# Kernel optimization log

Measured on AMD Instinct MI355X. Metric: run time of the kernel, lower is better.

## Reference

```python
import jax, jax.numpy as jnp
import numpy as np

NUM_HEAD = 16
HEAD_DIM = 64
D_MODEL = 1024


def setup_inputs() -> dict:
    key = jax.random.key(0)
    k_x, k_q, k_k, k_v, k_o, k_ob = jax.random.split(key, 6)
    B, T, D = 2, 2048, D_MODEL
    s = 1.0 / np.sqrt(D)
    return {
        "x": jax.random.normal(k_x, (B, T, D), dtype=jnp.float32),
        "Wq": jax.random.normal(k_q, (D, D), dtype=jnp.float32) * s,
        "Wk": jax.random.normal(k_k, (D, D), dtype=jnp.float32) * s,
        "Wv": jax.random.normal(k_v, (D, D), dtype=jnp.float32) * s,
        "Wo": jax.random.normal(k_o, (D, D), dtype=jnp.float32) * s,
        "bo": jax.random.normal(k_ob, (D,), dtype=jnp.float32) * 0.01,
    }


def reference(x, Wq, Wk, Wv, Wo, bo):
    B, T, D = x.shape
    H, Dh = NUM_HEAD, HEAD_DIM
    # Faithful to the source: W_query output is named `keys`, W_key output `queries`.
    keys = x @ Wq.T
    queries = x @ Wk.T
    values = x @ Wv.T
    # [B, T, D] -> [B, H, T, Dh]
    q = queries.reshape(B, T, H, Dh).transpose(0, 2, 1, 3)
    k = keys.reshape(B, T, H, Dh).transpose(0, 2, 1, 3)
    v = values.reshape(B, T, H, Dh).transpose(0, 2, 1, 3)
    scores = jnp.einsum("bhqd,bhkd->bhqk", q, k)
    causal = jnp.triu(jnp.ones((T, T), dtype=bool), k=1)  # True above diagonal -> masked
    scores = jnp.where(causal, -jnp.inf, scores)
    weights = jax.nn.softmax(scores / np.sqrt(Dh), axis=-1)
    # dropout p=0.0 (eval): identity
    ctx = jnp.einsum("bhqk,bhkd->bhqd", weights, v)
    ctx = ctx.transpose(0, 2, 1, 3).reshape(B, T, D)
    return ctx @ Wo.T + bo
```

## Files before the change

kernel.cpp:

```cpp
#include <hip/hip_runtime.h>

#define TT 2048
#define DD 1024
#define NH 16
#define DH 64
#define MR 4096

typedef __attribute__((ext_vector_type(8))) short bf16x8;
typedef __attribute__((ext_vector_type(4))) short bf16x4;
typedef __attribute__((ext_vector_type(4))) float f32x4;
typedef __attribute__((ext_vector_type(2))) unsigned int u32x2;

__device__ __forceinline__ float bf2f(unsigned short u) {
  unsigned int x = ((unsigned int)u) << 16;
  return __builtin_bit_cast(float, x);
}
__device__ __forceinline__ unsigned short f2bf(float f) {
  unsigned int x = __builtin_bit_cast(unsigned int, f);
  x = (x + 0x7fffu + ((x >> 16) & 1u)) >> 16;
  return (unsigned short)x;
}
__device__ __forceinline__ unsigned int pack_bf2(float a, float b) {
#if __has_builtin(__builtin_amdgcn_cvt_pk_bf16_f32)
  typedef __attribute__((ext_vector_type(2))) __bf16 bf2_t;
  bf2_t v = __builtin_amdgcn_cvt_pk_bf16_f32(a, b);
  return __builtin_bit_cast(unsigned int, v);
#else
  return (unsigned int)f2bf(a) | ((unsigned int)f2bf(b) << 16);
#endif
}
__device__ __forceinline__ bf16x8 load8(const float* p) {
  bf16x8 r;
#pragma unroll
  for (int e = 0; e < 8; ++e) r[e] = (short)f2bf(p[e]);
  return r;
}

#if __has_builtin(__builtin_amdgcn_mfma_f32_16x16x16_bf16)
#define MFMA_K16(A, B, C) __builtin_amdgcn_mfma_f32_16x16x16_bf16(A, B, C, 0, 0, 0)
#else
#define MFMA_K16(A, B, C) __builtin_amdgcn_mfma_f32_16x16x16bf16_1k(A, B, C, 0, 0, 0)
#endif

__device__ __forceinline__ void stage16(const unsigned short* g,
                                        unsigned short* lbase, int lane) {
#if __has_builtin(__builtin_amdgcn_global_load_lds)
  __builtin_amdgcn_global_load_lds(
      (const __attribute__((address_space(1))) unsigned int*)g,
      (__attribute__((address_space(3))) unsigned int*)(lbase + lane * 8),
      16, 0, 0);
#else
  *(bf16x8*)(lbase + lane * 8) = *(const bf16x8*)g;
#endif
}

__global__ __launch_bounds__(256) void cvt_all(
    const float* __restrict__ Wq, const float* __restrict__ Wk,
    const float* __restrict__ Wv, const float* __restrict__ Wo,
    const float* __restrict__ x,
    unsigned short* __restrict__ Wb, unsigned short* __restrict__ xb)
{
  int c = blockIdx.x * 256 + threadIdx.x;
  if (c < 524288) {
    int idx = c * 8, n = idx >> 10, col = idx & 1023;
    const float* src = (n < 1024) ? Wk + (size_t)n * 1024
                     : (n < 2048) ? Wq + (size_t)(n - 1024) * 1024
                     : (n < 3072) ? Wv + (size_t)(n - 2048) * 1024
                                  : Wo + (size_t)(n - 3072) * 1024;
    *(bf16x8*)&Wb[idx] = load8(src + col);
  } else {
    size_t idx = (size_t)(c - 524288) * 8;
    *(bf16x8*)&xb[idx] = load8(&x[idx]);
  }
}

template <bool FAST>
__global__ __launch_bounds__(256) void gemm_qkv(
    const float* __restrict__ x, const unsigned short* __restrict__ xb,
    const unsigned short* __restrict__ Wb,
    unsigned short* __restrict__ Q, unsigned short* __restrict__ Kb,
    unsigned short* __restrict__ Vt)
{
  __shared__ unsigned short pool[8704];
  unsigned short* As = pool;
  unsigned short* Bs = pool + 4096;

  const int tid = threadIdx.x, wave = tid >> 6, lane = tid & 63;
  const int lr = lane & 15, quad = lane >> 4;
  const int bm = blockIdx.x * 128, bn = blockIdx.y * 128;
  const int wm = (wave >> 1) * 64, wn = (wave & 1) * 64;

  f32x4 acc[4][4] = {};

  for (int k0 = 0; k0 < 1024; k0 += 32) {
#pragma unroll
    for (int i = 0; i < 2; ++i) {
      int c = wave * 128 + i * 64 + lane;
      int row = c >> 2, l8 = (c & 3) ^ ((row >> 1) & 3);
      stage16(&Wb[(size_t)(bn + row) * 1024 + k0 + l8 * 8],
              &Bs[(wave * 2 + i) * 512], lane);
      if constexpr (FAST)
        stage16(&xb[(size_t)(bm + row) * 1024 + k0 + l8 * 8],
                &As[(wave * 2 + i) * 512], lane);
    }
    if constexpr (!FAST) {
#pragma unroll
      for (int i = 0; i < 2; ++i) {
        int c = tid + i * 256;
        int row = c >> 2, l8 = c & 3, p8 = l8 ^ ((row >> 1) & 3);
        *(bf16x8*)&As[row * 32 + p8 * 8] =
            load8(&x[(size_t)(bm + row) * 1024 + k0 + l8 * 8]);
      }
    }
    __syncthreads();

    bf16x8 af[4], bf[4];
#pragma unroll
    for (int mt = 0; mt < 4; ++mt) {
      int row = wm + mt * 16 + lr;
      af[mt] = *(const bf16x8*)&As[row * 32 + (quad ^ ((row >> 1) & 3)) * 8];
    }
#pragma unroll
    for (int nt = 0; nt < 4; ++nt) {
      int row = wn + nt * 16 + lr;
      bf[nt] = *(const bf16x8*)&Bs[row * 32 + (quad ^ ((row >> 1) & 3)) * 8];
    }
#pragma unroll
    for (int mt = 0; mt < 4; ++mt)
#pragma unroll
      for (int nt = 0; nt < 4; ++nt)
        acc[mt][nt] = __builtin_amdgcn_mfma_f32_16x16x32_bf16(
            af[mt], bf[nt], acc[mt][nt], 0, 0, 0);
    __syncthreads();
  }

  if (bn < 2048) {
    unsigned short* Cp = (bn < 1024) ? Q : Kb;
    int coff = (bn < 1024) ? bn : bn - 1024;
#pragma unroll
    for (int nt = 0; nt < 4; ++nt) {
      int col = coff + wn + nt * 16 + lr;
#pragma unroll
      for (int mt = 0; mt < 4; ++mt) {
        int row = bm + wm + mt * 16 + quad * 4;
#pragma unroll
        for (int r = 0; r < 4; ++r)
          Cp[(size_t)(row + r) * 1024 + col] = f2bf(acc[mt][nt][r]);
      }
    }
  } else {
    const int b = bm >> 11, t0 = bm & 2047, d0 = bn - 2048;
    unsigned short* Tt = pool;
#pragma unroll
    for (int hv = 0; hv < 2; ++hv) {
      __syncthreads();
      if ((wave & 1) == hv) {
#pragma unroll
        for (int nt = 0; nt < 4; ++nt)
#pragma unroll
          for (int mt = 0; mt < 4; ++mt)
#pragma unroll
            for (int r = 0; r < 4; ++r)
              Tt[(nt * 16 + lr) * 136 + wm + mt * 16 + quad * 4 + r] =
                  f2bf(acc[mt][nt][r]);
      }
      __syncthreads();
#pragma unroll
      for (int ch = 0; ch < 4; ++ch) {
        int cc = tid + ch * 256;
        int d64 = cc >> 4, t8 = cc & 15;
        int dg = d0 + hv * 64 + d64;
        int h = dg >> 6, d = dg & 63;
        bf16x8 v = *(const bf16x8*)&Tt[d64 * 136 + t8 * 8];
        *(bf16x8*)&Vt[(((size_t)(b * NH + h) * 64 + d) << 11) + t0 + t8 * 8] = v;
      }
    }
  }
}

__global__ __launch_bounds__(256) void attn(
    const unsigned short* __restrict__ Q,
    const unsigned short* __restrict__ Kb,
    const unsigned short* __restrict__ Vt,
    unsigned short* __restrict__ ctx)
{
  __shared__ unsigned short Ks[128 * 64];
  __shared__ unsigned short Vs[64 * 128];

  const int tid = threadIdx.x, wave = tid >> 6, lane = tid & 63;
  const int lr = lane & 15, quad = lane >> 4;
  const int p = blockIdx.x & 15;
  const int h = (blockIdx.x >> 4) & 15;
  const int b = blockIdx.x >> 8;

  const size_t qkbase = ((size_t)b * TT) * 1024 + h * 64;
  const size_t vbase  = ((size_t)(b * NH + h) * 64) << 11;
  const float QS = 0.125f * 1.44269504f;

  bf16x4 ones;
#pragma unroll
  for (int e = 0; e < 4; ++e) ones[e] = (short)0x3F80;

#pragma unroll
  for (int pass = 0; pass < 2; ++pass) {
    const int qt = pass ? p : (31 - p);
    const int qrow0 = qt * 64 + wave * 16;
    const int qrow  = qrow0 + lr;

    bf16x8 qf[2];
#pragma unroll
    for (int kb = 0; kb < 2; ++kb) {
      bf16x8 raw = *(const bf16x8*)&Q[qkbase + (size_t)(qrow0 + lr) * 1024 + kb * 32 + quad * 8];
#pragma unroll
      for (int e = 0; e < 8; ++e)
        qf[kb][e] = (short)f2bf(bf2f((unsigned short)raw[e]) * QS);
    }

    float m_i = -1e30f;
    f32x4 od[4] = {};
    f32x4 ol = {};
    const int jmax = qt >> 1;

    for (int j = 0; j <= jmax; ++j) {
#pragma unroll
      for (int i = 0; i < 4; ++i) {
        int ci = (wave * 4 + i) * 64 + lane;
        int row = ci >> 3, lc = (ci & 7) ^ (row & 7);
        stage16(&Kb[qkbase + (size_t)(j * 128 + row) * 1024 + lc * 8],
                &Ks[(wave * 4 + i) * 512], lane);
      }
#pragma unroll
      for (int i = 0; i < 4; ++i) {
        int ci = (wave * 4 + i) * 64 + lane;
        int d = ci >> 4, lc = (ci & 15) ^ (d & 15);
        stage16(&Vt[vbase + ((size_t)d << 11) + j * 128 + lc * 8],
                &Vs[(wave * 4 + i) * 512], lane);
      }
      __syncthreads();

      const bool diag = (j == jmax);
      const int nlim = (diag && !(qt & 1)) ? 4 : 8;

      f32x4 s[8];
#pragma unroll
      for (int nt = 0; nt < 8; ++nt)
        if (nt < nlim) {
          f32x4 a = {0.f, 0.f, 0.f, 0.f};
#pragma unroll
          for (int kb = 0; kb < 2; ++kb) {
            int pc = (kb * 4 + quad) ^ (lr & 7);
            bf16x8 kf = *(const bf16x8*)&Ks[(nt * 16 + lr) * 64 + pc * 8];
            a = __builtin_amdgcn_mfma_f32_16x16x32_bf16(kf, qf[kb], a, 0, 0, 0);
          }
          s[nt] = a;
        }

      if (diag) {
#pragma unroll
        for (int nt = 0; nt < 8; ++nt)
          if (nt < nlim)
#pragma unroll
            for (int r = 0; r < 4; ++r) {
              int kpos = j * 128 + nt * 16 + quad * 4 + r;
              if (kpos > qrow) s[nt][r] = -1e30f;
            }
      }

      float mloc = -1e30f;
#pragma unroll
      for (int nt = 0; nt < 8; ++nt)
        if (nt < nlim)
#pragma unroll
          for (int r = 0; r < 4; ++r) mloc = fmaxf(mloc, s[nt][r]);
      mloc = fmaxf(mloc, __shfl_xor(mloc, 16, 64));
      mloc = fmaxf(mloc, __shfl_xor(mloc, 32, 64));
      float mnew = fmaxf(m_i, mloc);
      float alpha = exp2f(m_i - mnew);
      m_i = mnew;

      bf16x4 pk[8];
#pragma unroll
      for (int nt = 0; nt < 8; ++nt)
        if (nt < nlim) {
          float p0 = exp2f(s[nt][0] - mnew), p1 = exp2f(s[nt][1] - mnew);
          float p2 = exp2f(s[nt][2] - mnew), p3 = exp2f(s[nt][3] - mnew);
          u32x2 u = {pack_bf2(p0, p1), pack_bf2(p2, p3)};
          pk[nt] = __builtin_bit_cast(bf16x4, u);
        }

      float am[4];
#pragma unroll
      for (int r = 0; r < 4; ++r) am[r] = __shfl(alpha, quad * 4 + r, 16);
#pragma unroll
      for (int dt = 0; dt < 4; ++dt)
#pragma unroll
        for (int r = 0; r < 4; ++r) od[dt][r] *= am[r];
#pragma unroll
      for (int r = 0; r < 4; ++r) ol[r] *= am[r];

#pragma unroll
      for (int nt = 0; nt < 8; ++nt)
        if (nt < nlim) {
#pragma unroll
          for (int dt = 0; dt < 4; ++dt) {
            int pc = (nt * 2 + (quad >> 1)) ^ lr;
            bf16x4 vf = *(const bf16x4*)&Vs[(dt * 16 + lr) * 128 + pc * 8 + (quad & 1) * 4];
            od[dt] = MFMA_K16(pk[nt], vf, od[dt]);
          }
          ol = MFMA_K16(pk[nt], ones, ol);
        }
      __syncthreads();
    }

#pragma unroll
    for (int dt = 0; dt < 4; ++dt) {
      int col = h * 64 + dt * 16 + lr;
#pragma unroll
      for (int r = 0; r < 4; ++r) {
        int row = qrow0 + quad * 4 + r;
        ctx[((size_t)b * TT + row) * 1024 + col] = f2bf(od[dt][r] / ol[r]);
      }
    }
  }
}

__global__ __launch_bounds__(256) void gemm_out(
    const unsigned short* __restrict__ A,
    const unsigned short* __restrict__ Bw,
    const float* __restrict__ bias,
    float* __restrict__ out)
{
  __shared__ unsigned short pool[8192];
  unsigned short* As = pool;
  unsigned short* Bs = pool + 4096;

  const int tid = threadIdx.x, wave = tid >> 6, lane = tid & 63;
  const int lr = lane & 15, quad = lane >> 4;
  const int bm = blockIdx.x * 128, bn = blockIdx.y * 128;
  const int wm = (wave >> 1) * 64, wn = (wave & 1) * 64;

  f32x4 acc[4][4] = {};

  for (int k0 = 0; k0 < 1024; k0 += 32) {
#pragma unroll
    for (int i = 0; i < 2; ++i) {
      int c = wave * 128 + i * 64 + lane;
      int row = c >> 2, l8 = (c & 3) ^ ((row >> 1) & 3);
      stage16(&A[(size_t)(bm + row) * 1024 + k0 + l8 * 8],
              &As[(wave * 2 + i) * 512], lane);
      stage16(&Bw[(size_t)(bn + row) * 1024 + k0 + l8 * 8],
              &Bs[(wave * 2 + i) * 512], lane);
    }
    __syncthreads();

    bf16x8 af[4], bf[4];
#pragma unroll
    for (int mt = 0; mt < 4; ++mt) {
      int row = wm + mt * 16 + lr;
      af[mt] = *(const bf16x8*)&As[row * 32 + (quad ^ ((row >> 1) & 3)) * 8];
    }
#pragma unroll
    for (int nt = 0; nt < 4; ++nt) {
      int row = wn + nt * 16 + lr;
      bf[nt] = *(const bf16x8*)&Bs[row * 32 + (quad ^ ((row >> 1) & 3)) * 8];
    }
#pragma unroll
    for (int mt = 0; mt < 4; ++mt)
#pragma unroll
      for (int nt = 0; nt < 4; ++nt)
        acc[mt][nt] = __builtin_amdgcn_mfma_f32_16x16x32_bf16(
            af[mt], bf[nt], acc[mt][nt], 0, 0, 0);
    __syncthreads();
  }

#pragma unroll
  for (int nt = 0; nt < 4; ++nt) {
    int col = bn + wn + nt * 16 + lr;
    float bv = bias[col];
#pragma unroll
    for (int mt = 0; mt < 4; ++mt) {
      int row = bm + wm + mt * 16 + quad * 4;
#pragma unroll
      for (int r = 0; r < 4; ++r)
        out[(size_t)(row + r) * 1024 + col] = acc[mt][nt][r] + bv;
    }
  }
}

extern "C" void kernel_launch(void* const* d_in, const int* in_sizes, int n_in,
                              void* d_out, int out_size, void* d_ws, size_t ws_size,
                              hipStream_t stream) {
  const float* x  = (const float*)d_in[0];
  const float* Wq = (const float*)d_in[1];
  const float* Wk = (const float*)d_in[2];
  const float* Wv = (const float*)d_in[3];
  const float* Wo = (const float*)d_in[4];
  const float* bo = (const float*)d_in[5];
  float* out = (float*)d_out;
  unsigned short* ws = (unsigned short*)d_ws;

  const size_t SZ = (size_t)MR * DD;

  unsigned short* Qb  = ws;
  unsigned short* Kbf = ws + SZ;
  unsigned short* Vt  = ws + 2 * SZ;
  unsigned short* Wb  = ws + 3 * SZ;
  unsigned short* xb  = ws + 4 * SZ;

  const bool fast = ws_size >= 5 * SZ * sizeof(unsigned short);

  cvt_all<<<dim3(fast ? 4096 : 2048), 256, 0, stream>>>(Wq, Wk, Wv, Wo, x, Wb, xb);
  if (fast)
    gemm_qkv<true><<<dim3(32, 24), 256, 0, stream>>>(x, xb, Wb, Qb, Kbf, Vt);
  else
    gemm_qkv<false><<<dim3(32, 24), 256, 0, stream>>>(x, xb, Wb, Qb, Kbf, Vt);
  attn<<<dim3(2 * NH * 16), 256, 0, stream>>>(Qb, Kbf, Vt, Qb);
  gemm_out<<<dim3(32, 8), 256, 0, stream>>>(Qb, Wb + 3 * (size_t)DD * DD, bo, out);
}
```

Before: 197.3 us.

## Double-buffer K/V tiles and process 128 query rows per attention block

Each attention block now covers 128 query rows as two 64-row groups per wave, reusing each staged K/V tile for twice as many queries, and the grid is halved. K/V tiles are double-buffered in shared memory, with the next tile staged before computing on the current one to overlap loads with math. This costs double the LDS footprint, more registers for two sets of accumulators, and fewer resident waves per CU.

```diff
diff --git a/kernel.cpp b/kernel.cpp
--- a/kernel.cpp
+++ b/kernel.cpp
@@ -178,20 +178,20 @@
   }
 }
 
-__global__ __launch_bounds__(256) void attn(
+__global__ __launch_bounds__(256, 1) void attn(
     const unsigned short* __restrict__ Q,
     const unsigned short* __restrict__ Kb,
     const unsigned short* __restrict__ Vt,
     unsigned short* __restrict__ ctx)
 {
-  __shared__ unsigned short Ks[128 * 64];
-  __shared__ unsigned short Vs[64 * 128];
+  __shared__ unsigned short Ks[2 * 128 * 64];
+  __shared__ unsigned short Vs[2 * 64 * 128];
 
   const int tid = threadIdx.x, wave = tid >> 6, lane = tid & 63;
   const int lr = lane & 15, quad = lane >> 4;
-  const int p = blockIdx.x & 15;
-  const int h = (blockIdx.x >> 4) & 15;
-  const int b = blockIdx.x >> 8;
+  const int p = blockIdx.x & 7;
+  const int h = (blockIdx.x >> 3) & 15;
+  const int b = blockIdx.x >> 7;
 
   const size_t qkbase = ((size_t)b * TT) * 1024 + h * 64;
   const size_t vbase  = ((size_t)(b * NH + h) * 64) << 11;
@@ -201,126 +201,143 @@
 #pragma unroll
   for (int e = 0; e < 4; ++e) ones[e] = (short)0x3F80;
 
+  auto stage_kv = [&](int j, int bf) {
+#pragma unroll
+    for (int i = 0; i < 4; ++i) {
+      int ci = (wave * 4 + i) * 64 + lane;
+      int row = ci >> 3, lc = (ci & 7) ^ (row & 7);
+      stage16(&Kb[qkbase + (size_t)(j * 128 + row) * 1024 + lc * 8],
+              &Ks[bf * 8192 + (wave * 4 + i) * 512], lane);
+    }
+#pragma unroll
+    for (int i = 0; i < 4; ++i) {
+      int ci = (wave * 4 + i) * 64 + lane;
+      int d = ci >> 4, lc = (ci & 15) ^ (d & 15);
+      stage16(&Vt[vbase + ((size_t)d << 11) + j * 128 + lc * 8],
+              &Vs[bf * 8192 + (wave * 4 + i) * 512], lane);
+    }
+  };
+
 #pragma unroll
   for (int pass = 0; pass < 2; ++pass) {
-    const int qt = pass ? p : (31 - p);
-    const int qrow0 = qt * 64 + wave * 16;
-    const int qrow  = qrow0 + lr;
-
-    bf16x8 qf[2];
-#pragma unroll
-    for (int kb = 0; kb < 2; ++kb) {
-      bf16x8 raw = *(const bf16x8*)&Q[qkbase + (size_t)(qrow0 + lr) * 1024 + kb * 32 + quad * 8];
-#pragma unroll
-      for (int e = 0; e < 8; ++e)
-        qf[kb][e] = (short)f2bf(bf2f((unsigned short)raw[e]) * QS);
-    }
-
-    float m_i = -1e30f;
-    f32x4 od[4] = {};
-    f32x4 ol = {};
-    const int jmax = qt >> 1;
+    const int qt = pass ? p : (15 - p);
+    const int q0 = qt * 128 + wave * 16;
+    const int jmax = qt;
+
+    bf16x8 qf[2][2];
+#pragma unroll
+    for (int g = 0; g < 2; ++g)
+#pragma unroll
+      for (int kb = 0; kb < 2; ++kb) {
+        bf16x8 raw = *(const bf16x8*)&Q[qkbase +
+            (size_t)(q0 + g * 64 + lr) * 1024 + kb * 32 + quad * 8];
+#pragma unroll
+        for (int e = 0; e < 8; ++e)
+          qf[g][kb][e] = (short)f2bf(bf2f((unsigned short)raw[e]) * QS);
+      }
+
+    float m_i[2] = {-1e30f, -1e30f};
+    f32x4 od[2][4] = {};
+    f32x4 ol[2] = {};
+
+    stage_kv(0, 0);
+    __syncthreads();
 
     for (int j = 0; j <= jmax; ++j) {
-#pragma unroll
-      for (int i = 0; i < 4; ++i) {
-        int ci = (wave * 4 + i) * 64 + lane;
-        int row = ci >> 3, lc = (ci & 7) ^ (row & 7);
-        stage16(&Kb[qkbase + (size_t)(j * 128 + row) * 1024 + lc * 8],
-                &Ks[(wave * 4 + i) * 512], lane);
-      }
-#pragma unroll
-      for (int i = 0; i < 4; ++i) {
-        int ci = (wave * 4 + i) * 64 + lane;
-        int d = ci >> 4, lc = (ci & 15) ^ (d & 15);
-        stage16(&Vt[vbase + ((size_t)d << 11) + j * 128 + lc * 8],
-                &Vs[(wave * 4 + i) * 512], lane);
-      }
-      __syncthreads();
-
+      const int buf = j & 1;
+      if (j < jmax) stage_kv(j + 1, buf ^ 1);
       const bool diag = (j == jmax);
-      const int nlim = (diag && !(qt & 1)) ? 4 : 8;
-
-      f32x4 s[8];
-#pragma unroll
-      for (int nt = 0; nt < 8; ++nt)
-        if (nt < nlim) {
-          f32x4 a = {0.f, 0.f, 0.f, 0.f};
-#pragma unroll
-          for (int kb = 0; kb < 2; ++kb) {
-            int pc = (kb * 4 + quad) ^ (lr & 7);
-            bf16x8 kf = *(const bf16x8*)&Ks[(nt * 16 + lr) * 64 + pc * 8];
-            a = __builtin_amdgcn_mfma_f32_16x16x32_bf16(kf, qf[kb], a, 0, 0, 0);
-          }
-          s[nt] = a;
+
+      f32x4 s[2][8];
+#pragma unroll
+      for (int nt = 0; nt < 8; ++nt) {
+        f32x4 a0 = {0.f, 0.f, 0.f, 0.f}, a1 = a0;
+        const bool need0 = !diag || nt < 4;
+#pragma unroll
+        for (int kb = 0; kb < 2; ++kb) {
+          int pc = (kb * 4 + quad) ^ (lr & 7);
+          bf16x8 kf = *(const bf16x8*)&Ks[buf * 8192 + (nt * 16 + lr) * 64 + pc * 8];
+          if (need0)
+            a0 = __builtin_amdgcn_mfma_f32_16x16x32_bf16(kf, qf[0][kb], a0, 0, 0, 0);
+          a1 = __builtin_amdgcn_mfma_f32_16x16x32_bf16(kf, qf[1][kb], a1, 0, 0, 0);
         }
-
-      if (diag) {
+        s[0][nt] = a0; s[1][nt] = a1;
+      }
+
+      bf16x4 pk[2][8];
+      float alpha[2];
+#pragma unroll
+      for (int g = 0; g < 2; ++g) {
+        const int nlim = (diag && g == 0) ? 4 : 8;
+        const int qrow = q0 + g * 64 + lr;
+        if (diag) {
+#pragma unroll
+          for (int nt = 0; nt < 8; ++nt)
+            if (nt < nlim)
+#pragma unroll
+              for (int r = 0; r < 4; ++r) {
+                int kpos = j * 128 + nt * 16 + quad * 4 + r;
+                if (kpos > qrow) s[g][nt][r] = -1e30f;
+              }
+        }
+        float mloc = -1e30f;
 #pragma unroll
         for (int nt = 0; nt < 8; ++nt)
           if (nt < nlim)
 #pragma unroll
-            for (int r = 0; r < 4; ++r) {
-              int kpos = j * 128 + nt * 16 + quad * 4 + r;
-              if (kpos > qrow) s[nt][r] = -1e30f;
-            }
-      }
-
-      float mloc = -1e30f;
-#pragma unroll
-      for (int nt = 0; nt < 8; ++nt)
-        if (nt < nlim)
-#pragma unroll
-          for (int r = 0; r < 4; ++r) mloc = fmaxf(mloc, s[nt][r]);
-      mloc = fmaxf(mloc, __shfl_xor(mloc, 16, 64));
-      mloc = fmaxf(mloc, __shfl_xor(mloc, 32, 64));
-      float mnew = fmaxf(m_i, mloc);
-      float alpha = exp2f(m_i - mnew);
-      m_i = mnew;
-
-      bf16x4 pk[8];
-#pragma unroll
-      for (int nt = 0; nt < 8; ++nt)
-        if (nt < nlim) {
-          float p0 = exp2f(s[nt][0] - mnew), p1 = exp2f(s[nt][1] - mnew);
-          float p2 = exp2f(s[nt][2] - mnew), p3 = exp2f(s[nt][3] - mnew);
-          u32x2 u = {pack_bf2(p0, p1), pack_bf2(p2, p3)};
-          pk[nt] = __builtin_bit_cast(bf16x4, u);
+            for (int r = 0; r < 4; ++r) mloc = fmaxf(mloc, s[g][nt][r]);
+        mloc = fmaxf(mloc, __shfl_xor(mloc, 16, 64));
+        mloc = fmaxf(mloc, __shfl_xor(mloc, 32, 64));
+        float mnew = fmaxf(m_i[g], mloc);
+        alpha[g] = exp2f(m_i[g] - mnew);
+        m_i[g] = mnew;
+#pragma unroll
+        for (int nt = 0; nt < 8; ++nt)
+          if (nt < nlim) {
+            float p0 = exp2f(s[g][nt][0] - mnew), p1 = exp2f(s[g][nt][1] - mnew);
+            float p2 = exp2f(s[g][nt][2] - mnew), p3 = exp2f(s[g][nt][3] - mnew);
+            u32x2 u = {pack_bf2(p0, p1), pack_bf2(p2, p3)};
+            pk[g][nt] = __builtin_bit_cast(bf16x4, u);
+          }
+        float am[4];
+#pragma unroll
+        for (int r = 0; r < 4; ++r) am[r] = __shfl(alpha[g], quad * 4 + r, 16);
+#pragma unroll
+        for (int dt = 0; dt < 4; ++dt)
+#pragma unroll
+          for (int r = 0; r < 4; ++r) od[g][dt][r] *= am[r];
+#pragma unroll
+        for (int r = 0; r < 4; ++r) ol[g][r] *= am[r];
+      }
+
+#pragma unroll
+      for (int nt = 0; nt < 8; ++nt) {
+        const bool need0 = !diag || nt < 4;
+#pragma unroll
+        for (int dt = 0; dt < 4; ++dt) {
+          int pc = (nt * 2 + (quad >> 1)) ^ lr;
+          bf16x4 vf = *(const bf16x4*)&Vs[buf * 8192 +
+              (dt * 16 + lr) * 128 + pc * 8 + (quad & 1) * 4];
+          if (need0) od[0][dt] = MFMA_K16(pk[0][nt], vf, od[0][dt]);
+          od[1][dt] = MFMA_K16(pk[1][nt], vf, od[1][dt]);
         }
-
-      float am[4];
-#pragma unroll
-      for (int r = 0; r < 4; ++r) am[r] = __shfl(alpha, quad * 4 + r, 16);
-#pragma unroll
-      for (int dt = 0; dt < 4; ++dt)
-#pragma unroll
-        for (int r = 0; r < 4; ++r) od[dt][r] *= am[r];
-#pragma unroll
-      for (int r = 0; r < 4; ++r) ol[r] *= am[r];
-
-#pragma unroll
-      for (int nt = 0; nt < 8; ++nt)
-        if (nt < nlim) {
-#pragma unroll
-          for (int dt = 0; dt < 4; ++dt) {
-            int pc = (nt * 2 + (quad >> 1)) ^ lr;
-            bf16x4 vf = *(const bf16x4*)&Vs[(dt * 16 + lr) * 128 + pc * 8 + (quad & 1) * 4];
-            od[dt] = MFMA_K16(pk[nt], vf, od[dt]);
-          }
-          ol = MFMA_K16(pk[nt], ones, ol);
+        if (need0) ol[0] = MFMA_K16(pk[0][nt], ones, ol[0]);
+        ol[1] = MFMA_K16(pk[1][nt], ones, ol[1]);
+      }
+      __syncthreads();
+    }
+
+#pragma unroll
+    for (int g = 0; g < 2; ++g)
+#pragma unroll
+      for (int dt = 0; dt < 4; ++dt) {
+        int col = h * 64 + dt * 16 + lr;
+#pragma unroll
+        for (int r = 0; r < 4; ++r) {
+          int row = q0 + g * 64 + quad * 4 + r;
+          ctx[((size_t)b * TT + row) * 1024 + col] = f2bf(od[g][dt][r] / ol[g][r]);
         }
-      __syncthreads();
-    }
-
-#pragma unroll
-    for (int dt = 0; dt < 4; ++dt) {
-      int col = h * 64 + dt * 16 + lr;
-#pragma unroll
-      for (int r = 0; r < 4; ++r) {
-        int row = qrow0 + quad * 4 + r;
-        ctx[((size_t)b * TT + row) * 1024 + col] = f2bf(od[dt][r] / ol[r]);
-      }
-    }
+      }
   }
 }
 
@@ -414,6 +431,6 @@
     gemm_qkv<true><<<dim3(32, 24), 256, 0, stream>>>(x, xb, Wb, Qb, Kbf, Vt);
   else
     gemm_qkv<false><<<dim3(32, 24), 256, 0, stream>>>(x, xb, Wb, Qb, Kbf, Vt);
-  attn<<<dim3(2 * NH * 16), 256, 0, stream>>>(Qb, Kbf, Vt, Qb);
+  attn<<<dim3(2 * NH * 8), 256, 0, stream>>>(Qb, Kbf, Vt, Qb);
   gemm_out<<<dim3(32, 8), 256, 0, stream>>>(Qb, Wb + 3 * (size_t)DD * DD, bo, out);
 }
```

Result: slower. 212.0 us (+7.5%).
